# Performance work log

Measured on AMD Instinct MI355X. Metric: run time of the kernel, lower is better.

## Reference

```python
import jax, jax.numpy as jnp
import numpy as np
import math

VOCAB, D, H, NL, L, B = 50257, 768, 12, 4, 1024, 2
DH = D // H
DFF = 4 * D
ALPHA = 0.25
NEG = -1e9


def _ln(x, g, b, eps=1e-5):
    mu = x.mean(-1, keepdims=True)
    var = ((x - mu) ** 2).mean(-1, keepdims=True)
    return (x - mu) * jax.lax.rsqrt(var + eps) * g + b


def setup_inputs() -> dict:
    key = jax.random.key(0)
    ks = jax.random.split(key, 16)
    s = 0.02
    tokens = jax.random.randint(ks[0], (B, L), 0, VOCAB)
    timelike_mask = jax.random.randint(ks[1], (NL, D), 0, 2).astype(jnp.int32)
    embed = jax.random.normal(ks[2], (VOCAB, D), jnp.float32) * s
    pos_emb = jax.random.normal(ks[3], (L, D), jnp.float32) * s
    wq = jax.random.normal(ks[4], (NL, D, D), jnp.float32) * s
    wk = jax.random.normal(ks[5], (NL, D, D), jnp.float32) * s
    wv = jax.random.normal(ks[6], (NL, D, D), jnp.float32) * s
    wo = jax.random.normal(ks[7], (NL, D, D), jnp.float32) * s
    ff_w1 = jax.random.normal(ks[8], (NL, DFF, D), jnp.float32) * s
    ff_b1 = jnp.zeros((NL, DFF), jnp.float32)
    ff_w2 = jax.random.normal(ks[9], (NL, D, DFF), jnp.float32) * s
    ff_b2 = jnp.zeros((NL, D), jnp.float32)
    ln1_g = jnp.ones((NL, D), jnp.float32); ln1_b = jnp.zeros((NL, D), jnp.float32)
    ln2_g = jnp.ones((NL, D), jnp.float32); ln2_b = jnp.zeros((NL, D), jnp.float32)
    lnf_g = jnp.ones((D,), jnp.float32); lnf_b = jnp.zeros((D,), jnp.float32)
    return dict(tokens=tokens, timelike_mask=timelike_mask, embed=embed, pos_emb=pos_emb,
                wq=wq, wk=wk, wv=wv, wo=wo,
                ln1_g=ln1_g, ln1_b=ln1_b, ln2_g=ln2_g, ln2_b=ln2_b,
                ff_w1=ff_w1, ff_b1=ff_b1, ff_w2=ff_w2, ff_b2=ff_b2,
                lnf_g=lnf_g, lnf_b=lnf_b)


def reference(tokens, timelike_mask, embed, pos_emb, wq, wk, wv, wo,
              ln1_g, ln1_b, ln2_g, ln2_b, ff_w1, ff_b1, ff_w2, ff_b2,
              lnf_g, lnf_b):
    Bc, Lc = tokens.shape
    scale = math.sqrt(DH)
    # embeddings: token + learned position
    h = embed[tokens] + pos_emb[None, :Lc]  # (B,L,D)
    # additive causal mask, matching torch's -inf attention_mask convention
    causal = jnp.where(jnp.tril(jnp.ones((Lc, Lc), bool)), 0.0, NEG)[None, None]  # (1,1,L,L)
    for i in range(NL):
        xn = _ln(h, ln1_g[i], ln1_b[i])
        # nn.Linear(bias=False): y = x @ W.T, W is (out,in)
        q = jnp.einsum('bld,od->blo', xn, wq[i]).reshape(Bc, Lc, H, DH).astype(jnp.float32)
        k = jnp.einsum('bld,od->blo', xn, wk[i]).reshape(Bc, Lc, H, DH).astype(jnp.float32)
        v = jnp.einsum('bld,od->blo', xn, wv[i]).reshape(Bc, Lc, H, DH)
        # Minkowski term: scores_std - 2*alpha*(Q*P_t)K^T  ==  (Q*(1-2*alpha*m)) K^T
        m = timelike_mask[i].astype(jnp.float32).reshape(H, DH)  # per-head timelike directions
        q_eff = q * (1.0 - 2.0 * ALPHA * m)[None, None]
        scores = jnp.einsum('bqhd,bkhd->bhqk', q_eff, k) / scale + causal
        aw = jax.nn.softmax(scores, axis=-1)  # dropout=0 (eval)
        attn = jnp.einsum('bhqk,bkhd->bqhd', aw, v).reshape(Bc, Lc, D)
        h = h + jnp.einsum('bld,od->blo', attn, wo[i])
        xn2 = _ln(h, ln2_g[i], ln2_b[i])
        ff = jax.nn.gelu(jnp.einsum('bld,fd->blf', xn2, ff_w1[i]) + ff_b1[i], approximate=False)
        h = h + jnp.einsum('blf,df->bld', ff, ff_w2[i]) + ff_b2[i]
    h = _ln(h, lnf_g, lnf_b)
    logits = jnp.einsum('bld,vd->blv', h, embed)  # tied LM head
    return logits
```

## Files before the change

kernel.cpp:

```cpp
#include <hip/hip_runtime.h>
#include <math.h>

#define VOCABSZ 50257
#define VPAD 50432
#define DMODEL 768
#define NHEAD 12
#define NLAYER 4
#define SEQ 1024
#define BATCH 2
#define DHEAD 64
#define DFFN 3072
#define BT (BATCH * SEQ)
#define NBH (BATCH * NHEAD)

typedef __attribute__((ext_vector_type(8))) short bf16x8;
typedef __attribute__((ext_vector_type(4))) float f32x4;

__device__ __forceinline__ ushort f2bf(float f) {
  uint u = __builtin_bit_cast(uint, f);
  u = (u + 0x7fffu + ((u >> 16) & 1u)) >> 16;
  return (ushort)u;
}

__device__ __forceinline__ void gl_lds16(const ushort* g, ushort* l) {
  __builtin_amdgcn_global_load_lds(
      (const __attribute__((address_space(1))) void*)g,
      (__attribute__((address_space(3))) void*)l, 16, 0, 0);
}

__global__ __launch_bounds__(256) void conv4_kernel(
    const float* __restrict__ src, ushort* __restrict__ dst, int n4) {
  int i = blockIdx.x * 256 + threadIdx.x;
  if (i >= n4) return;
  float4 v = reinterpret_cast<const float4*>(src)[i];
  reinterpret_cast<ushort4*>(dst)[i] =
      make_ushort4(f2bf(v.x), f2bf(v.y), f2bf(v.z), f2bf(v.w));
}

__global__ __launch_bounds__(256) void conv_qkv_kernel(
    const float* __restrict__ src, ushort* __restrict__ dst, int qoff4) {
  const int per4 = DMODEL * DMODEL / 4;
  int i = blockIdx.x * 256 + threadIdx.x;
  if (i >= NLAYER * per4) return;
  int layer = i / per4, rem = i % per4;
  float4 v = reinterpret_cast<const float4*>(src)[i];
  reinterpret_cast<ushort4*>(dst)[(size_t)layer * (3 * per4) + qoff4 + rem] =
      make_ushort4(f2bf(v.x), f2bf(v.y), f2bf(v.z), f2bf(v.w));
}

__global__ __launch_bounds__(256) void conv_embed_kernel(
    const float* __restrict__ emb, ushort* __restrict__ dst) {
  int i = blockIdx.x * 256 + threadIdx.x;
  if (i >= VPAD * DMODEL / 4) return;
  int row = (i * 4) / DMODEL;
  ushort4 o = make_ushort4(0, 0, 0, 0);
  if (row < VOCABSZ) {
    float4 v = reinterpret_cast<const float4*>(emb)[i];
    o = make_ushort4(f2bf(v.x), f2bf(v.y), f2bf(v.z), f2bf(v.w));
  }
  reinterpret_cast<ushort4*>(dst)[i] = o;
}

__global__ __launch_bounds__(256) void embed_kernel(
    const int* __restrict__ tok, const float* __restrict__ emb,
    const float* __restrict__ pos, float* __restrict__ h) {
  int row = blockIdx.x;
  int l = row % SEQ;
  int t = tok[row];
  int tid = threadIdx.x;
#pragma unroll
  for (int j = 0; j < 3; ++j) {
    int c = tid + j * 256;
    h[(size_t)row * DMODEL + c] =
        emb[(size_t)t * DMODEL + c] + pos[(size_t)l * DMODEL + c];
  }
}

template <int KS, bool RBIAS>
__global__ __launch_bounds__(256) void ln_kernel(
    float* __restrict__ h, const float* __restrict__ part,
    const float* __restrict__ rb, const float* __restrict__ g,
    const float* __restrict__ bta, ushort* __restrict__ o) {
  __shared__ float red[8];
  int row = blockIdx.x;
  int tid = threadIdx.x;
  float* xr = h + (size_t)row * DMODEL;
  float v[3];
  float s = 0.f, sq = 0.f;
#pragma unroll
  for (int j = 0; j < 3; ++j) {
    int c = tid + j * 256;
    float a = xr[c];
    if (RBIAS) a += rb[c];
    if (KS > 0) {
#pragma unroll
      for (int z = 0; z < KS; ++z)
        a += part[(size_t)z * BT * DMODEL + (size_t)row * DMODEL + c];
      xr[c] = a;
    }
    v[j] = a;
    s += a;
    sq += a * a;
  }
#pragma unroll
  for (int off = 1; off < 64; off <<= 1) {
    s += __shfl_xor(s, off);
    sq += __shfl_xor(sq, off);
  }
  int wid = tid >> 6;
  if ((tid & 63) == 0) { red[wid * 2] = s; red[wid * 2 + 1] = sq; }
  __syncthreads();
  float S = red[0] + red[2] + red[4] + red[6];
  float SQ = red[1] + red[3] + red[5] + red[7];
  float mu = S * (1.0f / DMODEL);
  float var = SQ * (1.0f / DMODEL) - mu * mu;
  float r = rsqrtf(var + 1e-5f);
  ushort* orow = o + (size_t)row * DMODEL;
#pragma unroll
  for (int j = 0; j < 3; ++j) {
    int c = tid + j * 256;
    orow[c] = f2bf((v[j] - mu) * r * g[c] + bta[c]);
  }
}

__global__ __launch_bounds__(256) void fattn_kernel(
    const ushort* __restrict__ q, const ushort* __restrict__ k,
    const ushort* __restrict__ vt, ushort* __restrict__ o) {
  __shared__ __align__(16) ushort Ks[64 * 64];
  __shared__ __align__(16) ushort Vs[64 * 64];
  __shared__ __align__(16) ushort Ps[4][16][80];
  const int z = blockIdx.y, b = z / NHEAD, hh = z % NHEAD;
  const int q0 = (gridDim.x - 1 - blockIdx.x) * 64;
  const int tid = threadIdx.x, w = tid >> 6, l = tid & 63;
  const int fr = l & 15, ks = l >> 4;
  const int qrow = q0 + w * 16 + fr;
  const ushort* qp = q + (size_t)(b * SEQ + qrow) * DMODEL + hh * DHEAD;
  const bf16x8 qf0 = *reinterpret_cast<const bf16x8*>(qp + ks * 8);
  const bf16x8 qf1 = *reinterpret_cast<const bf16x8*>(qp + 32 + ks * 8);

  const int srow = w * 16 + (l >> 3);
  const int sslot = l & 7;

  f32x4 acc_o[4] = {};
  float mrun = -1e30f, lrun = 0.f;

  for (int k0 = 0; k0 <= q0; k0 += 64) {
#pragma unroll
    for (int c = 0; c < 2; ++c) {
      int r = srow + c * 8;
      int g = sslot ^ (r & 7);
      gl_lds16(k + (size_t)(b * SEQ + k0 + r) * DMODEL + hh * DHEAD + g * 8,
               Ks + (w * 16 + c * 8) * 64);
      gl_lds16(vt + (size_t)(z * 64 + r) * SEQ + k0 + g * 8,
               Vs + (w * 16 + c * 8) * 64);
    }
    __syncthreads();
    f32x4 acc_s[4] = {};
#pragma unroll
    for (int kstep = 0; kstep < 2; ++kstep) {
      const bf16x8 qf = kstep ? qf1 : qf0;
#pragma unroll
      for (int kb = 0; kb < 4; ++kb) {
        int ra = kb * 16 + fr;
        bf16x8 af = *reinterpret_cast<const bf16x8*>(
            Ks + ra * 64 + (((kstep * 4 + ks) ^ (ra & 7)) * 8));
        acc_s[kb] =
            __builtin_amdgcn_mfma_f32_16x16x32_bf16(af, qf, acc_s[kb], 0, 0, 0);
      }
    }
    const bool diag = (k0 == q0);
    float pm = -1e30f;
    float sv[4][4];
#pragma unroll
    for (int kb = 0; kb < 4; ++kb)
#pragma unroll
      for (int r = 0; r < 4; ++r) {
        float s = acc_s[kb][r];
        if (diag && (k0 + kb * 16 + ks * 4 + r > qrow)) s = -1e30f;
        sv[kb][r] = s;
        pm = fmaxf(pm, s);
      }
    pm = fmaxf(pm, __shfl_xor(pm, 16));
    pm = fmaxf(pm, __shfl_xor(pm, 32));
    float mnew = fmaxf(mrun, pm);
    float scale = __expf(mrun - mnew);
    float psum = 0.f;
#pragma unroll
    for (int kb = 0; kb < 4; ++kb) {
      float p0 = __expf(sv[kb][0] - mnew);
      float p1 = __expf(sv[kb][1] - mnew);
      float p2 = __expf(sv[kb][2] - mnew);
      float p3 = __expf(sv[kb][3] - mnew);
      psum += (p0 + p1) + (p2 + p3);
      *reinterpret_cast<ushort4*>(&Ps[w][fr][kb * 16 + ks * 4]) =
          make_ushort4(f2bf(p0), f2bf(p1), f2bf(p2), f2bf(p3));
    }
    psum += __shfl_xor(psum, 16);
    psum += __shfl_xor(psum, 32);
    lrun = lrun * scale + psum;
    mrun = mnew;
#pragma unroll
    for (int db = 0; db < 4; ++db) acc_o[db] *= scale;
#pragma unroll
    for (int kstep = 0; kstep < 2; ++kstep) {
      bf16x8 pf =
          *reinterpret_cast<const bf16x8*>(&Ps[w][fr][kstep * 32 + ks * 8]);
#pragma unroll
      for (int db = 0; db < 4; ++db) {
        int rd = db * 16 + fr;
        bf16x8 vf = *reinterpret_cast<const bf16x8*>(
            Vs + rd * 64 + (((kstep * 4 + ks) ^ (rd & 7)) * 8));
        acc_o[db] =
            __builtin_amdgcn_mfma_f32_16x16x32_bf16(vf, pf, acc_o[db], 0, 0, 0);
      }
    }
    __syncthreads();
  }
  float rinv = 1.0f / lrun;
#pragma unroll
  for (int db = 0; db < 4; ++db) {
    ushort4 o4 =
        make_ushort4(f2bf(acc_o[db][0] * rinv), f2bf(acc_o[db][1] * rinv),
                     f2bf(acc_o[db][2] * rinv), f2bf(acc_o[db][3] * rinv));
    *reinterpret_cast<ushort4*>(o + (size_t)(b * SEQ + qrow) * DMODEL +
                                hh * DHEAD + db * 16 + ks * 4) = o4;
  }
}

template <bool QKV, bool BIAS, bool GELU, bool RES, bool OUTBF, bool SWZ,
          bool PART>
__global__ __launch_bounds__(256) void gemm_bf16_nt(
    const ushort* __restrict__ A, const ushort* __restrict__ B,
    const float* __restrict__ bias, const int* __restrict__ tmask,
    const float* __restrict__ res, float* __restrict__ Cf,
    ushort* __restrict__ Cb, int ldc, ushort* __restrict__ qb,
    ushort* __restrict__ kb, ushort* __restrict__ vt, int M, int K, int Nreal,
    int kchunk) {
  __shared__ __align__(16) ushort As[2][128 * 32];
  __shared__ __align__(16) ushort Bs[2][128 * 32];
  int bnx, bmy;
  if (SWZ) {
    int bid = blockIdx.x;
    int chunk = gridDim.x >> 3;
    int wgid = (bid & 7) * chunk + (bid >> 3);
    int mb = M >> 7;
    bmy = wgid % mb;
    bnx = wgid / mb;
  } else {
    bnx = blockIdx.x;
    bmy = blockIdx.y;
  }
  const int m0 = bmy * 128, n0 = bnx * 128;
  const int kbeg = PART ? blockIdx.z * kchunk : 0;
  const int kend = PART ? kbeg + kchunk : K;
  if (PART) Cf += (size_t)blockIdx.z * M * ldc;
  const int tid = threadIdx.x;
  const int w = tid >> 6, l = tid & 63;
  const int wr = w >> 1, wc = w & 1;
  const int fr = l & 15, ks = l >> 4;

  const int seg0 = w * 2, seg1 = w * 2 + 1;
  const int srow0 = seg0 * 16 + (l >> 2);
  const int srow1 = seg1 * 16 + (l >> 2);
  const int koff0 = (((l & 3) ^ ((srow0 >> 1) & 3))) * 8;
  const int koff1 = (((l & 3) ^ ((srow1 >> 1) & 3))) * 8;
  const ushort* A0 = A + (size_t)(m0 + srow0) * K + koff0;
  const ushort* A1 = A + (size_t)(m0 + srow1) * K + koff1;
  const ushort* B0 = B + (size_t)(n0 + srow0) * K + koff0;
  const ushort* B1 = B + (size_t)(n0 + srow1) * K + koff1;

  int aoff[4], boff[4];
#pragma unroll
  for (int i = 0; i < 4; ++i) {
    int ra = wr * 64 + i * 16 + fr;
    aoff[i] = ra * 32 + ((ks ^ ((ra >> 1) & 3)) * 8);
    int rb = wc * 64 + i * 16 + fr;
    boff[i] = rb * 32 + ((ks ^ ((rb >> 1) & 3)) * 8);
  }

  gl_lds16(A0 + kbeg, &As[0][seg0 * 512]);
  gl_lds16(A1 + kbeg, &As[0][seg1 * 512]);
  gl_lds16(B0 + kbeg, &Bs[0][seg0 * 512]);
  gl_lds16(B1 + kbeg, &Bs[0][seg1 * 512]);

  f32x4 acc[4][4] = {};
  int cur = 0;
  for (int k0 = kbeg; k0 < kend; k0 += 32) {
    const int nxt = k0 + 32;
    if (nxt < kend) {
      gl_lds16(A0 + nxt, &As[cur ^ 1][seg0 * 512]);
      gl_lds16(A1 + nxt, &As[cur ^ 1][seg1 * 512]);
      gl_lds16(B0 + nxt, &Bs[cur ^ 1][seg0 * 512]);
      gl_lds16(B1 + nxt, &Bs[cur ^ 1][seg1 * 512]);
      asm volatile("s_waitcnt vmcnt(4)" ::: "memory");
    } else {
      asm volatile("s_waitcnt vmcnt(0)" ::: "memory");
    }
    __builtin_amdgcn_s_barrier();
    __builtin_amdgcn_sched_barrier(0);
    bf16x8 af[4], bfr[4];
#pragma unroll
    for (int i = 0; i < 4; ++i)
      af[i] = *reinterpret_cast<const bf16x8*>(&As[cur][aoff[i]]);
#pragma unroll
    for (int i = 0; i < 4; ++i)
      bfr[i] = *reinterpret_cast<const bf16x8*>(&Bs[cur][boff[i]]);
#pragma unroll
    for (int mi = 0; mi < 4; ++mi)
#pragma unroll
      for (int nj = 0; nj < 4; ++nj)
        acc[mi][nj] = __builtin_amdgcn_mfma_f32_16x16x32_bf16(
            af[mi], bfr[nj], acc[mi][nj], 0, 0, 0);
    __builtin_amdgcn_sched_barrier(0);
    __builtin_amdgcn_s_barrier();
    cur ^= 1;
  }

#pragma unroll
  for (int mi = 0; mi < 4; ++mi) {
#pragma unroll
    for (int nj = 0; nj < 4; ++nj) {
      int n = n0 + wc * 64 + nj * 16 + fr;
      if (n < Nreal) {
        if (PART) {
#pragma unroll
          for (int r = 0; r < 4; ++r) {
            int m = m0 + wr * 64 + mi * 16 + ks * 4 + r;
            Cf[(size_t)m * ldc + n] = acc[mi][nj][r];
          }
        } else if (QKV) {
          if (n < DMODEL) {
            float sc = (1.0f - 0.5f * (float)tmask[n]) * 0.125f;
#pragma unroll
            for (int r = 0; r < 4; ++r) {
              int m = m0 + wr * 64 + mi * 16 + ks * 4 + r;
              qb[(size_t)m * DMODEL + n] = f2bf(acc[mi][nj][r] * sc);
            }
          } else if (n < 2 * DMODEL) {
#pragma unroll
            for (int r = 0; r < 4; ++r) {
              int m = m0 + wr * 64 + mi * 16 + ks * 4 + r;
              kb[(size_t)m * DMODEL + (n - DMODEL)] = f2bf(acc[mi][nj][r]);
            }
          } else {
            int d = n - 2 * DMODEL;
            int key = (m0 & (SEQ - 1)) + wr * 64 + mi * 16 + ks * 4;
            size_t zr = (size_t)((m0 >> 10) * NHEAD + (d >> 6)) * 64 + (d & 63);
            ushort4 p4 = make_ushort4(
                f2bf(acc[mi][nj][0]), f2bf(acc[mi][nj][1]),
                f2bf(acc[mi][nj][2]), f2bf(acc[mi][nj][3]));
            *reinterpret_cast<ushort4*>(vt + zr * SEQ + key) = p4;
          }
        } else {
#pragma unroll
          for (int r = 0; r < 4; ++r) {
            int m = m0 + wr * 64 + mi * 16 + ks * 4 + r;
            float v = acc[mi][nj][r];
            if (BIAS) v += bias[n];
            if (GELU) v = 0.5f * v * (1.0f + erff(v * 0.70710678118f));
            if (RES) v += res[(size_t)m * ldc + n];
            if (OUTBF)
              Cb[(size_t)m * ldc + n] = f2bf(v);
            else
              Cf[(size_t)m * ldc + n] = v;
          }
        }
      }
    }
  }
}

__global__ __launch_bounds__(512, 2) void gemm_lmhead(
    const ushort* __restrict__ A, const ushort* __restrict__ B,
    float* __restrict__ C) {
  __shared__ __align__(16) ushort SMEM[4 * 256 * 64];
  const int K = DMODEL;
  const int NTILE = K / 64;
  const int ITERS = NTILE / 2;

  const int bid = blockIdx.x;
  const int chunk = gridDim.x >> 3;
  const int wgid = (bid & 7) * chunk + (bid >> 3);
  const int m0 = (wgid & 7) * 256;
  const int n0 = (wgid >> 3) * 256;

  const int tid = threadIdx.x;
  const int w = tid >> 6, l = tid & 63;
  const int wr = w >> 2, wc = w & 3;
  const int fr = l & 15, ks = l >> 4;

  const int strow = tid >> 3;
  const int stk = ((tid & 7) ^ (strow & 7)) * 8;
  const int wseg = (w << 3) * 64;

  const int fsw0 = (ks ^ (fr & 7)) * 8;
  const int fsw1 = ((4 | ks) ^ (fr & 7)) * 8;
  const int arow = (wr * 128 + fr) * 64;
  const int brow = (wc * 64 + fr) * 64;

  bf16x8 Ar[4][2], Br[4][2];
  f32x4 acc[8][4] = {};

#define STA(d, kt, rb)                                            \
  gl_lds16(A + (size_t)(m0 + (rb) + strow) * K + (kt) * 64 + stk, \
           SMEM + (d) * 16384 + (rb) * 64 + wseg)
#define STB(d, kt, rb)                                            \
  gl_lds16(B + (size_t)(n0 + (rb) + strow) * K + (kt) * 64 + stk, \
           SMEM + 32768 + (d) * 16384 + (rb) * 64 + wseg)
#define RDA(d, mi, kst)                           \
  (*reinterpret_cast<const bf16x8*>(              \
      &SMEM[(d) * 16384 + arow + (mi) * 1024 + ((kst) ? fsw1 : fsw0)]))
#define RDB(d, nj, kst)                           \
  (*reinterpret_cast<const bf16x8*>(              \
      &SMEM[32768 + (d) * 16384 + brow + (nj) * 1024 + ((kst) ? fsw1 : fsw0)]))
#define MMAQ(mh, nh)                                                       \
  _Pragma("unroll") for (int kst = 0; kst < 2; ++kst)                      \
  _Pragma("unroll") for (int mi = 0; mi < 4; ++mi)                         \
  _Pragma("unroll") for (int nj = 0; nj < 2; ++nj)                         \
    acc[(mh)*4 + mi][(nh)*2 + nj] = __builtin_amdgcn_mfma_f32_16x16x32_bf16( \
        Ar[mi][kst], Br[(nh)*2 + nj][kst], acc[(mh)*4 + mi][(nh)*2 + nj],  \
        0, 0, 0)
#define BAR __builtin_amdgcn_s_barrier()
#define PRIO1 __builtin_amdgcn_s_setprio(1)
#define PRIO0 __builtin_amdgcn_s_setprio(0)

  STA(0, 0, 0); STA(0, 0, 64); STA(0, 0, 128); STA(0, 0, 192);
  STB(0, 0, 0); STB(0, 0, 64); STB(0, 0, 128); STB(0, 0, 192);
  STB(1, 1, 0); STB(1, 1, 64); STB(1, 1, 128); STB(1, 1, 192);
  asm volatile("s_waitcnt vmcnt(4)" ::: "memory");
  BAR;

  for (int it = 0; it < ITERS; ++it) {
    const int t1 = 2 * it + 1;
    const int tn = 2 * it + 2;
    const bool s0 = tn < NTILE, s1 = tn + 1 < NTILE;
#pragma unroll
    for (int mi = 0; mi < 4; ++mi) {
      Ar[mi][0] = RDA(0, mi, 0); Ar[mi][1] = RDA(0, mi, 1);
    }
#pragma unroll
    for (int nj = 0; nj < 2; ++nj) {
      Br[nj][0] = RDB(0, nj, 0); Br[nj][1] = RDB(0, nj, 1);
    }
    STA(1, t1, 0); STA(1, t1, 64);
    BAR; PRIO1; MMAQ(0, 0); PRIO0; BAR;
#pragma unroll
    for (int nj = 2; nj < 4; ++nj) {
      Br[nj][0] = RDB(0, nj, 0); Br[nj][1] = RDB(0, nj, 1);
    }
    STA(1, t1, 128); STA(1, t1, 192);
    BAR; PRIO1; MMAQ(0, 1); PRIO0; BAR;
#pragma unroll
    for (int mi = 0; mi < 4; ++mi) {
      Ar[mi][0] = RDA(0, mi + 4, 0); Ar[mi][1] = RDA(0, mi + 4, 1);
    }
    if (s0) { STB(0, tn, 0); STB(0, tn, 64); }
    BAR; PRIO1; MMAQ(1, 1); PRIO0; BAR;
    if (s0) { STB(0, tn, 128); STB(0, tn, 192); }
    BAR; PRIO1; MMAQ(1, 0); PRIO0;
    if (s0)
      asm volatile("s_waitcnt vmcnt(4)" ::: "memory");
    else
      asm volatile("s_waitcnt vmcnt(0)" ::: "memory");
    BAR;
#pragma unroll
    for (int mi = 0; mi < 4; ++mi) {
      Ar[mi][0] = RDA(1, mi, 0); Ar[mi][1] = RDA(1, mi, 1);
    }
#pragma unroll
    for (int nj = 0; nj < 2; ++nj) {
      Br[nj][0] = RDB(1, nj, 0); Br[nj][1] = RDB(1, nj, 1);
    }
    if (s0) { STA(0, tn, 0); STA(0, tn, 64); }
    BAR; PRIO1; MMAQ(0, 0); PRIO0; BAR;
#pragma unroll
    for (int nj = 2; nj < 4; ++nj) {
      Br[nj][0] = RDB(1, nj, 0); Br[nj][1] = RDB(1, nj, 1);
    }
    if (s0) { STA(0, tn, 128); STA(0, tn, 192); }
    BAR; PRIO1; MMAQ(0, 1); PRIO0; BAR;
#pragma unroll
    for (int mi = 0; mi < 4; ++mi) {
      Ar[mi][0] = RDA(1, mi + 4, 0); Ar[mi][1] = RDA(1, mi + 4, 1);
    }
    if (s1) { STB(1, tn + 1, 0); STB(1, tn + 1, 64); }
    BAR; PRIO1; MMAQ(1, 1); PRIO0; BAR;
    if (s1) { STB(1, tn + 1, 128); STB(1, tn + 1, 192); }
    BAR; PRIO1; MMAQ(1, 0); PRIO0;
    if (it + 1 < ITERS) {
      asm volatile("s_waitcnt vmcnt(4)" ::: "memory");
      BAR;
    }
  }

  float* eb = reinterpret_cast<float*>(SMEM);
#pragma unroll 1
  for (int p = 0; p < 2; ++p) {
    __syncthreads();
    if (wr == p) {
#pragma unroll
      for (int mi = 0; mi < 8; ++mi)
#pragma unroll
        for (int nj = 0; nj < 4; ++nj)
#pragma unroll
          for (int r = 0; r < 4; ++r)
            eb[(mi * 16 + ks * 4 + r) * 256 + wc * 64 + nj * 16 + fr] =
                acc[mi][nj][r];
    }
    __syncthreads();
    const size_t rowbase = (size_t)(m0 + p * 128) * VOCABSZ + n0;
#pragma unroll 8
    for (int c = 0; c < 64; ++c) {
      int lin = c * 512 + tid;
      int row = lin >> 8, col = lin & 255;
      if (n0 + col < VOCABSZ) {
        __builtin_nontemporal_store(
            eb[lin], C + rowbase + (size_t)row * VOCABSZ + col);
      }
    }
  }
#undef STA
#undef STB
#undef RDA
#undef RDB
#undef MMAQ
#undef BAR
#undef PRIO1
#undef PRIO0
}

extern "C" void kernel_launch(void* const* d_in, const int* in_sizes, int n_in,
                              void* d_out, int out_size, void* d_ws,
                              size_t ws_size, hipStream_t stream) {
  const int* tokens = (const int*)d_in[0];
  const int* tmask = (const int*)d_in[1];
  const float* embed = (const float*)d_in[2];
  const float* pos = (const float*)d_in[3];
  const float* wq = (const float*)d_in[4];
  const float* wk = (const float*)d_in[5];
  const float* wv = (const float*)d_in[6];
  const float* wo = (const float*)d_in[7];
  const float* ln1g = (const float*)d_in[8];
  const float* ln1b = (const float*)d_in[9];
  const float* ln2g = (const float*)d_in[10];
  const float* ln2b = (const float*)d_in[11];
  const float* fw1 = (const float*)d_in[12];
  const float* fb1 = (const float*)d_in[13];
  const float* fw2 = (const float*)d_in[14];
  const float* fb2 = (const float*)d_in[15];
  const float* lnfg = (const float*)d_in[16];
  const float* lnfb = (const float*)d_in[17];

  char* wp = (char*)d_ws;
  auto alloc = [&](size_t bytes) {
    void* p = wp;
    wp += (bytes + 255) & ~(size_t)255;
    return p;
  };
  float* h = (float*)alloc((size_t)BT * DMODEL * 4);
  float* part = (float*)alloc((size_t)4 * BT * DMODEL * 4);
  ushort* qb = (ushort*)alloc((size_t)BT * DMODEL * 2);
  ushort* kb = (ushort*)alloc((size_t)BT * DMODEL * 2);
  ushort* vt = (ushort*)alloc((size_t)NBH * DHEAD * SEQ * 2);
  ushort* xn = (ushort*)alloc((size_t)BT * DMODEL * 2);
  ushort* ab = (ushort*)alloc((size_t)BT * DMODEL * 2);
  ushort* ffb = (ushort*)alloc((size_t)BT * DFFN * 2);
  ushort* wqkv_b = (ushort*)alloc((size_t)NLAYER * 3 * DMODEL * DMODEL * 2);
  ushort* wo_b = (ushort*)alloc((size_t)NLAYER * DMODEL * DMODEL * 2);
  ushort* fw1_b = (ushort*)alloc((size_t)NLAYER * DFFN * DMODEL * 2);
  ushort* fw2_b = (ushort*)alloc((size_t)NLAYER * DMODEL * DFFN * 2);
  ushort* emb_b = (ushort*)alloc((size_t)VPAD * DMODEL * 2);

  const int per4 = DMODEL * DMODEL / 4;
  conv_qkv_kernel<<<(NLAYER * per4 + 255) / 256, 256, 0, stream>>>(wq, wqkv_b, 0);
  conv_qkv_kernel<<<(NLAYER * per4 + 255) / 256, 256, 0, stream>>>(wk, wqkv_b, per4);
  conv_qkv_kernel<<<(NLAYER * per4 + 255) / 256, 256, 0, stream>>>(wv, wqkv_b, 2 * per4);
  conv4_kernel<<<(NLAYER * per4 + 255) / 256, 256, 0, stream>>>(wo, wo_b, NLAYER * per4);
  const int nff4 = NLAYER * DFFN * DMODEL / 4;
  conv4_kernel<<<(nff4 + 255) / 256, 256, 0, stream>>>(fw1, fw1_b, nff4);
  conv4_kernel<<<(nff4 + 255) / 256, 256, 0, stream>>>(fw2, fw2_b, nff4);
  conv_embed_kernel<<<(VPAD * DMODEL / 4 + 255) / 256, 256, 0, stream>>>(embed, emb_b);

  embed_kernel<<<BT, 256, 0, stream>>>(tokens, embed, pos, h);

  const dim3 gqkv(3 * DMODEL / 128, BT / 128);
  const dim3 gff(DFFN / 128, BT / 128);
  const dim3 gwo(DMODEL / 128, BT / 128, 2);
  const dim3 gff2(DMODEL / 128, BT / 128, 4);

  for (int i = 0; i < NLAYER; ++i) {
    if (i == 0)
      ln_kernel<0, false><<<BT, 256, 0, stream>>>(
          h, nullptr, nullptr, ln1g + i * DMODEL, ln1b + i * DMODEL, xn);
    else
      ln_kernel<4, true><<<BT, 256, 0, stream>>>(
          h, part, fb2 + (i - 1) * DMODEL, ln1g + i * DMODEL,
          ln1b + i * DMODEL, xn);

    gemm_bf16_nt<true, false, false, false, false, false, false>
        <<<gqkv, 256, 0, stream>>>(
            xn, wqkv_b + (size_t)i * 3 * DMODEL * DMODEL, nullptr,
            tmask + i * DMODEL, nullptr, nullptr, nullptr, 0, qb, kb, vt, BT,
            DMODEL, 3 * DMODEL, DMODEL);

    fattn_kernel<<<dim3(SEQ / 64, NBH), 256, 0, stream>>>(qb, kb, vt, ab);

    gemm_bf16_nt<false, false, false, false, false, false, true>
        <<<gwo, 256, 0, stream>>>(
            ab, wo_b + (size_t)i * DMODEL * DMODEL, nullptr, nullptr, nullptr,
            part, nullptr, DMODEL, nullptr, nullptr, nullptr, BT, DMODEL,
            DMODEL, DMODEL / 2);

    ln_kernel<2, false><<<BT, 256, 0, stream>>>(
        h, part, nullptr, ln2g + i * DMODEL, ln2b + i * DMODEL, xn);

    gemm_bf16_nt<false, true, true, false, true, false, false>
        <<<gff, 256, 0, stream>>>(
            xn, fw1_b + (size_t)i * DFFN * DMODEL, fb1 + i * DFFN, nullptr,
            nullptr, nullptr, ffb, DFFN, nullptr, nullptr, nullptr, BT, DMODEL,
            DFFN, DMODEL);

    gemm_bf16_nt<false, false, false, false, false, false, true>
        <<<gff2, 256, 0, stream>>>(
            ffb, fw2_b + (size_t)i * DMODEL * DFFN, nullptr, nullptr, nullptr,
            part, nullptr, DMODEL, nullptr, nullptr, nullptr, BT, DFFN, DMODEL,
            DFFN / 4);
  }

  ln_kernel<4, true><<<BT, 256, 0, stream>>>(
      h, part, fb2 + (NLAYER - 1) * DMODEL, lnfg, lnfb, xn);

  gemm_lmhead<<<8 * (VPAD / 256), 512, 0, stream>>>(xn, emb_b, (float*)d_out);
}
```

Baseline: 879.4 us.

## Double-buffer K/V tiles in flash attention, add lazy rescale and XCD-aware block mapping

The flash-attention kernel now double-buffers its K and V tiles in LDS, prefetching the next tile with explicit vmcnt waits so global loads overlap the MFMA work on the current tile. The online softmax skips the rescale of the running max and accumulators unless some row's max grows by more than 8, trading a little numerical headroom for fewer exp and multiply operations. The launch becomes a 1D grid whose block index is remapped so that blocks for the same head tend to land on the same XCD for better L2 reuse. Doubling the K/V buffers raises LDS use per block, which may lower occupancy.

```diff
diff --git a/kernel.cpp b/kernel.cpp
--- a/kernel.cpp
+++ b/kernel.cpp
@@ -126,11 +126,14 @@
 __global__ __launch_bounds__(256) void fattn_kernel(
     const ushort* __restrict__ q, const ushort* __restrict__ k,
     const ushort* __restrict__ vt, ushort* __restrict__ o) {
-  __shared__ __align__(16) ushort Ks[64 * 64];
-  __shared__ __align__(16) ushort Vs[64 * 64];
+  __shared__ __align__(16) ushort Ks[2][64 * 64];
+  __shared__ __align__(16) ushort Vs[2][64 * 64];
   __shared__ __align__(16) ushort Ps[4][16][80];
-  const int z = blockIdx.y, b = z / NHEAD, hh = z % NHEAD;
-  const int q0 = (gridDim.x - 1 - blockIdx.x) * 64;
+  const int bid = blockIdx.x;
+  const int wgid = (bid & 7) * 48 + (bid >> 3);
+  const int z = wgid / 16, qb_ = wgid % 16;
+  const int b = z / NHEAD, hh = z % NHEAD;
+  const int q0 = (15 - qb_) * 64;
   const int tid = threadIdx.x, w = tid >> 6, l = tid & 63;
   const int fr = l & 15, ks = l >> 4;
   const int qrow = q0 + w * 16 + fr;
@@ -139,22 +142,34 @@
   const bf16x8 qf1 = *reinterpret_cast<const bf16x8*>(qp + 32 + ks * 8);
 
   const int srow = w * 16 + (l >> 3);
-  const int sslot = l & 7;
+  const int g0 = ((l & 7) ^ (srow & 7)) * 8;
+
+  auto stage = [&](int k0, int d) {
+#pragma unroll
+    for (int c = 0; c < 2; ++c) {
+      int r = srow + c * 8;
+      gl_lds16(k + (size_t)(b * SEQ + k0 + r) * DMODEL + hh * DHEAD + g0,
+               &Ks[d][(w * 16 + c * 8) * 64]);
+      gl_lds16(vt + (size_t)(z * 64 + r) * SEQ + k0 + g0,
+               &Vs[d][(w * 16 + c * 8) * 64]);
+    }
+  };
 
   f32x4 acc_o[4] = {};
   float mrun = -1e30f, lrun = 0.f;
-
-  for (int k0 = 0; k0 <= q0; k0 += 64) {
-#pragma unroll
-    for (int c = 0; c < 2; ++c) {
-      int r = srow + c * 8;
-      int g = sslot ^ (r & 7);
-      gl_lds16(k + (size_t)(b * SEQ + k0 + r) * DMODEL + hh * DHEAD + g * 8,
-               Ks + (w * 16 + c * 8) * 64);
-      gl_lds16(vt + (size_t)(z * 64 + r) * SEQ + k0 + g * 8,
-               Vs + (w * 16 + c * 8) * 64);
-    }
-    __syncthreads();
+  const int nt = q0 >> 6;
+
+  stage(0, 0);
+  for (int t = 0; t <= nt; ++t) {
+    const int cur = t & 1;
+    if (t < nt) {
+      stage((t + 1) * 64, cur ^ 1);
+      asm volatile("s_waitcnt vmcnt(4)" ::: "memory");
+    } else {
+      asm volatile("s_waitcnt vmcnt(0)" ::: "memory");
+    }
+    __builtin_amdgcn_s_barrier();
+    __builtin_amdgcn_sched_barrier(0);
     f32x4 acc_s[4] = {};
 #pragma unroll
     for (int kstep = 0; kstep < 2; ++kstep) {
@@ -163,12 +178,12 @@
       for (int kb = 0; kb < 4; ++kb) {
         int ra = kb * 16 + fr;
         bf16x8 af = *reinterpret_cast<const bf16x8*>(
-            Ks + ra * 64 + (((kstep * 4 + ks) ^ (ra & 7)) * 8));
+            &Ks[cur][ra * 64 + (((kstep * 4 + ks) ^ (ra & 7)) * 8)]);
         acc_s[kb] =
             __builtin_amdgcn_mfma_f32_16x16x32_bf16(af, qf, acc_s[kb], 0, 0, 0);
       }
     }
-    const bool diag = (k0 == q0);
+    const bool diag = (t == nt);
     float pm = -1e30f;
     float sv[4][4];
 #pragma unroll
@@ -176,31 +191,34 @@
 #pragma unroll
       for (int r = 0; r < 4; ++r) {
         float s = acc_s[kb][r];
-        if (diag && (k0 + kb * 16 + ks * 4 + r > qrow)) s = -1e30f;
+        if (diag && (q0 + kb * 16 + ks * 4 + r > qrow)) s = -1e30f;
         sv[kb][r] = s;
         pm = fmaxf(pm, s);
       }
     pm = fmaxf(pm, __shfl_xor(pm, 16));
     pm = fmaxf(pm, __shfl_xor(pm, 32));
-    float mnew = fmaxf(mrun, pm);
-    float scale = __expf(mrun - mnew);
+    if (!__all(pm - mrun <= 8.0f)) {
+      float mnew = fmaxf(mrun, pm);
+      float scale = __expf(mrun - mnew);
+      lrun *= scale;
+#pragma unroll
+      for (int db = 0; db < 4; ++db) acc_o[db] *= scale;
+      mrun = mnew;
+    }
     float psum = 0.f;
 #pragma unroll
     for (int kb = 0; kb < 4; ++kb) {
-      float p0 = __expf(sv[kb][0] - mnew);
-      float p1 = __expf(sv[kb][1] - mnew);
-      float p2 = __expf(sv[kb][2] - mnew);
-      float p3 = __expf(sv[kb][3] - mnew);
+      float p0 = __expf(sv[kb][0] - mrun);
+      float p1 = __expf(sv[kb][1] - mrun);
+      float p2 = __expf(sv[kb][2] - mrun);
+      float p3 = __expf(sv[kb][3] - mrun);
       psum += (p0 + p1) + (p2 + p3);
       *reinterpret_cast<ushort4*>(&Ps[w][fr][kb * 16 + ks * 4]) =
           make_ushort4(f2bf(p0), f2bf(p1), f2bf(p2), f2bf(p3));
     }
     psum += __shfl_xor(psum, 16);
     psum += __shfl_xor(psum, 32);
-    lrun = lrun * scale + psum;
-    mrun = mnew;
-#pragma unroll
-    for (int db = 0; db < 4; ++db) acc_o[db] *= scale;
+    lrun += psum;
 #pragma unroll
     for (int kstep = 0; kstep < 2; ++kstep) {
       bf16x8 pf =
@@ -209,12 +227,13 @@
       for (int db = 0; db < 4; ++db) {
         int rd = db * 16 + fr;
         bf16x8 vf = *reinterpret_cast<const bf16x8*>(
-            Vs + rd * 64 + (((kstep * 4 + ks) ^ (rd & 7)) * 8));
+            &Vs[cur][rd * 64 + (((kstep * 4 + ks) ^ (rd & 7)) * 8)]);
         acc_o[db] =
             __builtin_amdgcn_mfma_f32_16x16x32_bf16(vf, pf, acc_o[db], 0, 0, 0);
       }
     }
-    __syncthreads();
+    __builtin_amdgcn_sched_barrier(0);
+    __builtin_amdgcn_s_barrier();
   }
   float rinv = 1.0f / lrun;
 #pragma unroll
@@ -603,7 +622,7 @@
             tmask + i * DMODEL, nullptr, nullptr, nullptr, 0, qb, kb, vt, BT,
             DMODEL, 3 * DMODEL, DMODEL);
 
-    fattn_kernel<<<dim3(SEQ / 64, NBH), 256, 0, stream>>>(qb, kb, vt, ab);
+    fattn_kernel<<<NBH * (SEQ / 64), 256, 0, stream>>>(qb, kb, vt, ab);
 
     gemm_bf16_nt<false, false, false, false, false, false, true>
         <<<gwo, 256, 0, stream>>>(
```

New measurement: 862.0 us. 2.0% less time.
